# Performance work log

Hardware: AMD Instinct MI355X
Metric: run time of the kernel (lower is better)

Reference implementation:

```python
import jax, jax.numpy as jnp
import numpy as np

SUBSPACE_DIMS = np.array([1, 3, 3, 1])  # grade dims of 3D Clifford algebra (8 blades)
NUM_FEAT, NUM_HEADS, N_TOKENS, BS, C = 16, 8, 2048, 4, 8


def mv_linear(x, w, b):
    # x: [B, in, 8]; w: [out, in, 4] -> repeat over subspace dims -> [out, in, 8]
    wfull = jnp.repeat(w, SUBSPACE_DIMS, axis=-1)
    out = jnp.einsum('bic,oic->boc', x, wfull)
    return out.at[:, :, 0].add(b)  # bias on scalar blade only


def setup_inputs() -> dict:
    key = jax.random.key(0)
    ks = jax.random.split(key, 9)
    s = 0.05
    return {
        'feature_matrix': jax.random.normal(ks[0], (BS * N_TOKENS, NUM_FEAT, C), jnp.float32),
        'attention_mask': jnp.zeros((BS, N_TOKENS, N_TOKENS), jnp.float32),
        'wq': jax.random.normal(ks[1], (NUM_FEAT * NUM_HEADS, NUM_FEAT, 4), jnp.float32) * s,
        'bq': jax.random.normal(ks[2], (NUM_FEAT * NUM_HEADS,), jnp.float32) * s,
        'wk': jax.random.normal(ks[3], (NUM_FEAT * NUM_HEADS, NUM_FEAT, 4), jnp.float32) * s,
        'bk': jax.random.normal(ks[4], (NUM_FEAT * NUM_HEADS,), jnp.float32) * s,
        'wv': jax.random.normal(ks[5], (NUM_FEAT * NUM_HEADS, NUM_FEAT, 4), jnp.float32) * s,
        'bv': jax.random.normal(ks[6], (NUM_FEAT * NUM_HEADS,), jnp.float32) * s,
        'wo': jax.random.normal(ks[7], (NUM_FEAT, NUM_FEAT * NUM_HEADS, 4), jnp.float32) * s,
        'bo': jax.random.normal(ks[8], (NUM_FEAT,), jnp.float32) * s,
    }


def reference(feature_matrix, attention_mask, wq, bq, wk, bk, wv, bv, wo, bo):
    H, D = NUM_HEADS, NUM_FEAT
    n = N_TOKENS
    bs = feature_matrix.shape[0] // n

    def split_heads(t):  # [(bs n), (h d), c] -> [bs, h, n, d*c]
        return t.reshape(bs, n, H, D, C).transpose(0, 2, 1, 3, 4).reshape(bs, H, n, D * C)

    q = split_heads(mv_linear(feature_matrix, wq, bq)) / jnp.sqrt(jnp.float32(D * 8))
    k = split_heads(mv_linear(feature_matrix, wk, bk))
    v = split_heads(mv_linear(feature_matrix, wv, bv))

    attn = jnp.einsum('bhqe,bhke->bhqk', q, k) + attention_mask[:, None, :, :]
    attn = jax.nn.softmax(attn, axis=-1)
    out = jnp.einsum('bhqk,bhke->bhqe', attn, v)  # [bs, H, n, D*C]

    # transpose(1,2) then view(bs*n, H*D, 8)
    out = out.transpose(0, 2, 1, 3).reshape(bs * n, H * D, C)
    return mv_linear(out, wo, bo)
```

## Files before the change

kernel.cpp:

```cpp
#include <hip/hip_runtime.h>
#include <hip/hip_bf16.h>

typedef __attribute__((ext_vector_type(8))) __bf16 bf16x8;
typedef __attribute__((ext_vector_type(4))) float f32x4;
typedef __attribute__((ext_vector_type(8))) unsigned short ushort8;

#define TOKS 8192
#define LOG2E 1.4426950408889634f

__global__ __launch_bounds__(128) void proj_kernel(
    const float* __restrict__ x,
    const float* __restrict__ wq, const float* __restrict__ bq,
    const float* __restrict__ wk, const float* __restrict__ bk,
    const float* __restrict__ wv, const float* __restrict__ bv,
    __bf16* __restrict__ Qg, __bf16* __restrict__ Kg, __bf16* __restrict__ Vg)
{
    __shared__ float xs[512];
    const int tid = threadIdx.x;
    const int t0 = blockIdx.x * 4;
    ((float4*)xs)[tid] = ((const float4*)(x + (size_t)t0 * 128))[tid];
    __syncthreads();
    const int o = tid, h = o >> 4, d = o & 15;

    float acc[3][4][8];
#pragma unroll
    for (int tz = 0; tz < 3; ++tz) {
        const float bias = (tz == 0 ? bq : tz == 1 ? bk : bv)[o];
#pragma unroll
        for (int t = 0; t < 4; ++t) {
            acc[tz][t][0] = bias;
#pragma unroll
            for (int c = 1; c < 8; ++c) acc[tz][t][c] = 0.f;
        }
    }
    const float4* w40 = (const float4*)(wq + o * 64);
    const float4* w41 = (const float4*)(wk + o * 64);
    const float4* w42 = (const float4*)(wv + o * 64);
    for (int i = 0; i < 16; ++i) {
        float4 wv3[3] = {w40[i], w41[i], w42[i]};
#pragma unroll
        for (int t = 0; t < 4; ++t) {
            f32x4 xlo = *(const f32x4*)(xs + t * 128 + i * 8);
            f32x4 xhi = *(const f32x4*)(xs + t * 128 + i * 8 + 4);
            float xv[8] = {xlo[0], xlo[1], xlo[2], xlo[3],
                           xhi[0], xhi[1], xhi[2], xhi[3]};
#pragma unroll
            for (int tz = 0; tz < 3; ++tz) {
                float wr[8] = {wv3[tz].x, wv3[tz].y, wv3[tz].y, wv3[tz].y,
                               wv3[tz].z, wv3[tz].z, wv3[tz].z, wv3[tz].w};
#pragma unroll
                for (int c = 0; c < 8; ++c) acc[tz][t][c] += xv[c] * wr[c];
            }
        }
    }
    const int bb = t0 >> 11, tt0 = t0 & 2047;
    size_t base = (((size_t)(bb * 8 + h)) * 2048 + tt0) * 128 + d * 8;
#pragma unroll
    for (int tz = 0; tz < 3; ++tz) {
        __bf16* Og = tz == 0 ? Qg : tz == 1 ? Kg : Vg;
        const float scale = (tz == 0) ? 0.08838834764831845f : 1.0f;
#pragma unroll
        for (int t = 0; t < 4; ++t) {
            bf16x8 v;
#pragma unroll
            for (int c = 0; c < 8; ++c) v[c] = (__bf16)(acc[tz][t][c] * scale);
            *(bf16x8*)(Og + base + (size_t)t * 128) = v;
        }
    }
}

__global__ __launch_bounds__(256) void transv_kernel(
    const __bf16* __restrict__ Vg, __bf16* __restrict__ Vt)
{
    __shared__ __align__(16) char T[16384];
    const int tid = threadIdx.x;
    const int bh = blockIdx.y, t0 = blockIdx.x * 64;
    const __bf16* src = Vg + ((size_t)bh * 2048 + t0) * 128;
#pragma unroll
    for (int it = 0; it < 4; ++it) {
        int cidx = it * 256 + tid;
        int r = cidx >> 4, e0 = (cidx & 15) * 8;
        bf16x8 v = *(const bf16x8*)(src + r * 128 + e0);
        *(bf16x8*)(T + ((r * 256 + e0 * 2) ^ ((r & 7) << 4))) = v;
    }
    __syncthreads();
    const int e = tid & 127, half = tid >> 7;
    __bf16* dst = Vt + ((size_t)bh * 128 + e) * 2048 + t0 + half * 32;
#pragma unroll
    for (int jc = 0; jc < 4; ++jc) {
        ushort8 o8;
#pragma unroll
        for (int j = 0; j < 8; ++j) {
            int t = half * 32 + jc * 8 + j;
            o8[j] = *(const unsigned short*)(T + ((t * 256 + e * 2) ^ ((t & 7) << 4)));
        }
        *(ushort8*)(dst + jc * 8) = o8;
    }
}

__global__ __launch_bounds__(256) void flash_kernel(
    const __bf16* __restrict__ Qg, const __bf16* __restrict__ Kg,
    const __bf16* __restrict__ Vtg, const float* __restrict__ mask,
    __bf16* __restrict__ AO)
{
    __shared__ __align__(16) char Kl[16384];
    __shared__ __align__(16) char Vl[16384];
    __shared__ __align__(16) char Pl[8192];

    const int tid = threadIdx.x;
    const int lane = tid & 63, w = tid >> 6;
    const int l15 = lane & 15, lg = lane >> 4;
    const int bh = blockIdx.y, b = bh >> 3;
    const int q0 = blockIdx.x * 64;

    int kg[4], klb[4], vg[4], vlb[4];
#pragma unroll
    for (int it = 0; it < 4; ++it) {
        int cidx = it * 256 + tid;
        int kv = cidx >> 4, c15 = cidx & 15;
        kg[it] = kv * 128 + c15 * 8;
        klb[it] = kv * 256 + ((c15 * 16) ^ ((kv & 7) << 4));
        int e = cidx >> 3, j = cidx & 7;
        vg[it] = e * 2048 + j * 8;
        vlb[it] = e * 128 + ((j * 16) ^ ((e & 7) << 4));
    }
    const __bf16* kbase = Kg + (size_t)bh * 2048 * 128;
    const __bf16* vtbase = Vtg + (size_t)bh * 128 * 2048;
    const float* mbase = mask + ((size_t)b * 2048 + q0 + w * 16 + l15) * 2048;

    bf16x8 qf[4];
    {
        const __bf16* qp = Qg + ((size_t)bh * 2048 + q0 + w * 16 + l15) * 128 + lg * 8;
#pragma unroll
        for (int ks = 0; ks < 4; ++ks) qf[ks] = *(const bf16x8*)(qp + ks * 32);
    }

    f32x4 o_acc[8];
#pragma unroll
    for (int i = 0; i < 8; ++i) o_acc[i] = (f32x4){0.f, 0.f, 0.f, 0.f};
    float m = -1e30f, lsum = 0.f;
    const int pbase = w * 2048 + l15 * 128;
    const int psw = (l15 & 7) << 4;

    bf16x8 kreg[4], vreg[4];
#pragma unroll
    for (int it = 0; it < 4; ++it) {
        kreg[it] = *(const bf16x8*)(kbase + kg[it]);
        vreg[it] = *(const bf16x8*)(vtbase + vg[it]);
    }
#pragma unroll
    for (int it = 0; it < 4; ++it) {
        *(bf16x8*)(Kl + klb[it]) = kreg[it];
        *(bf16x8*)(Vl + vlb[it]) = vreg[it];
    }
    f32x4 mr[4];
#pragma unroll
    for (int ct = 0; ct < 4; ++ct)
        mr[ct] = *(const f32x4*)(mbase + ct * 16 + lg * 4);

    for (int kv0 = 0; kv0 < 2048; kv0 += 64) {
        __syncthreads();
        const bool more = (kv0 + 64) < 2048;
        if (more) {
            const __bf16* kb = kbase + (size_t)(kv0 + 64) * 128;
            const __bf16* vb = vtbase + (kv0 + 64);
#pragma unroll
            for (int it = 0; it < 4; ++it) {
                kreg[it] = *(const bf16x8*)(kb + kg[it]);
                vreg[it] = *(const bf16x8*)(vb + vg[it]);
            }
        }

        f32x4 st[4];
        __builtin_amdgcn_s_setprio(1);
#pragma unroll
        for (int ct = 0; ct < 4; ++ct) {
            f32x4 acc = (f32x4){0.f, 0.f, 0.f, 0.f};
            const int kvr = ct * 16 + l15;
            const int rowb = kvr * 256, sw = (kvr & 7) << 4;
#pragma unroll
            for (int ks = 0; ks < 4; ++ks) {
                bf16x8 kf = *(const bf16x8*)(Kl + rowb + ((ks * 64 + lg * 16) ^ sw));
                acc = __builtin_amdgcn_mfma_f32_16x16x32_bf16(kf, qf[ks], acc, 0, 0, 0);
            }
            st[ct] = acc;
        }
        __builtin_amdgcn_s_setprio(0);
#pragma unroll
        for (int ct = 0; ct < 4; ++ct)
#pragma unroll
            for (int r = 0; r < 4; ++r) st[ct][r] += mr[ct][r];

        float pmax = fmaxf(fmaxf(fmaxf(st[0][0], st[0][1]), fmaxf(st[0][2], st[0][3])),
                           fmaxf(fmaxf(st[1][0], st[1][1]), fmaxf(st[1][2], st[1][3])));
        pmax = fmaxf(pmax,
               fmaxf(fmaxf(fmaxf(st[2][0], st[2][1]), fmaxf(st[2][2], st[2][3])),
                     fmaxf(fmaxf(st[3][0], st[3][1]), fmaxf(st[3][2], st[3][3]))));
        pmax = fmaxf(pmax, __shfl_xor(pmax, 16));
        pmax = fmaxf(pmax, __shfl_xor(pmax, 32));

        if (!__all(pmax - m <= 6.0f)) {
            const float mnew = fmaxf(m, pmax);
            const float alpha = exp2f((m - mnew) * LOG2E);
            m = mnew;
            lsum *= alpha;
#pragma unroll
            for (int ct2 = 0; ct2 < 8; ++ct2)
#pragma unroll
                for (int r = 0; r < 4; ++r) o_acc[ct2][r] *= alpha;
        }

        float rsum = 0.f;
#pragma unroll
        for (int ct = 0; ct < 4; ++ct) {
            union { __bf16 h[4]; unsigned long long u64; } pk;
#pragma unroll
            for (int r = 0; r < 4; ++r) {
                float p = exp2f((st[ct][r] - m) * LOG2E);
                rsum += p;
                pk.h[r] = (__bf16)p;
            }
            *(unsigned long long*)(Pl + pbase + ((ct * 32 + lg * 8) ^ psw)) = pk.u64;
        }
        rsum += __shfl_xor(rsum, 16);
        rsum += __shfl_xor(rsum, 32);
        lsum += rsum;

        asm volatile("s_waitcnt lgkmcnt(0)" ::: "memory");
        __builtin_amdgcn_sched_barrier(0);

        __builtin_amdgcn_s_setprio(1);
#pragma unroll
        for (int ks2 = 0; ks2 < 2; ++ks2) {
            bf16x8 pf = *(const bf16x8*)(Pl + pbase + ((ks2 * 64 + lg * 16) ^ psw));
#pragma unroll
            for (int ct2 = 0; ct2 < 8; ++ct2) {
                const int e = ct2 * 16 + l15;
                bf16x8 vf = *(const bf16x8*)(Vl + e * 128 +
                                             ((ks2 * 64 + lg * 16) ^ ((e & 7) << 4)));
                o_acc[ct2] = __builtin_amdgcn_mfma_f32_16x16x32_bf16(vf, pf, o_acc[ct2], 0, 0, 0);
            }
        }
        __builtin_amdgcn_s_setprio(0);
        __syncthreads();

        if (more) {
#pragma unroll
            for (int it = 0; it < 4; ++it) {
                *(bf16x8*)(Kl + klb[it]) = kreg[it];
                *(bf16x8*)(Vl + vlb[it]) = vreg[it];
            }
#pragma unroll
            for (int ct = 0; ct < 4; ++ct)
                mr[ct] = *(const f32x4*)(mbase + kv0 + 64 + ct * 16 + lg * 4);
        }
    }

    const float linv = 1.0f / lsum;
    const size_t tok = (size_t)b * 2048 + q0 + w * 16 + l15;
    __bf16* aop = AO + tok * 1024 + (bh & 7) * 128;
#pragma unroll
    for (int ct2 = 0; ct2 < 8; ++ct2) {
        union { __bf16 h[4]; unsigned long long u64; } ov;
#pragma unroll
        for (int r = 0; r < 4; ++r) ov.h[r] = (__bf16)(o_acc[ct2][r] * linv);
        *(unsigned long long*)(aop + ct2 * 16 + lg * 4) = ov.u64;
    }
}

__global__ __launch_bounds__(128) void outproj_kernel(
    const __bf16* __restrict__ AO, const float* __restrict__ wo,
    const float* __restrict__ bo, float* __restrict__ out)
{
    __shared__ float al[8 * 1032];
    const int tid = threadIdx.x;
    const int t0 = blockIdx.x * 8;
#pragma unroll
    for (int it = 0; it < 8; ++it) {
        bf16x8 v = *(const bf16x8*)(AO + (size_t)(t0 + it) * 1024 + tid * 8);
        f32x4 lo = {(float)v[0], (float)v[1], (float)v[2], (float)v[3]};
        f32x4 hi = {(float)v[4], (float)v[5], (float)v[6], (float)v[7]};
        *(f32x4*)(al + it * 1032 + tid * 8) = lo;
        *(f32x4*)(al + it * 1032 + tid * 8 + 4) = hi;
    }
    __syncthreads();
    const int o = tid >> 3, t = tid & 7;
    float acc[8];
    acc[0] = bo[o];
#pragma unroll
    for (int c = 1; c < 8; ++c) acc[c] = 0.f;
    const float4* w4 = (const float4*)wo + o * 128;
    for (int ii = 0; ii < 128; ++ii) {
        float4 wv = w4[ii];
        f32x4 xlo = *(const f32x4*)(al + t * 1032 + ii * 8);
        f32x4 xhi = *(const f32x4*)(al + t * 1032 + ii * 8 + 4);
        float wr[8] = {wv.x, wv.y, wv.y, wv.y, wv.z, wv.z, wv.z, wv.w};
        float xv[8] = {xlo[0], xlo[1], xlo[2], xlo[3], xhi[0], xhi[1], xhi[2], xhi[3]};
#pragma unroll
        for (int c = 0; c < 8; ++c) acc[c] += xv[c] * wr[c];
    }
    float* op = out + (size_t)(t0 + t) * 128 + o * 8;
    *(float4*)op = (float4){acc[0], acc[1], acc[2], acc[3]};
    *(float4*)(op + 4) = (float4){acc[4], acc[5], acc[6], acc[7]};
}

extern "C" void kernel_launch(void* const* d_in, const int* in_sizes, int n_in,
                              void* d_out, int out_size, void* d_ws, size_t ws_size,
                              hipStream_t stream)
{
    const float* x    = (const float*)d_in[0];
    const float* mask = (const float*)d_in[1];
    const float* wq   = (const float*)d_in[2];
    const float* bq   = (const float*)d_in[3];
    const float* wk   = (const float*)d_in[4];
    const float* bk   = (const float*)d_in[5];
    const float* wv   = (const float*)d_in[6];
    const float* bv   = (const float*)d_in[7];
    const float* wo   = (const float*)d_in[8];
    const float* bo   = (const float*)d_in[9];
    float* out = (float*)d_out;

    const size_t SLOT = (size_t)32 * 2048 * 128;
    const size_t need = SLOT * 4 * 2;
    if (ws_size < need) {
        hipMemsetAsync(d_out, 0, (size_t)out_size * sizeof(float), stream);
        return;
    }
    __bf16* Qg = (__bf16*)d_ws;
    __bf16* Kg = Qg + SLOT;
    __bf16* Vg = Kg + SLOT;
    __bf16* Vt = Vg + SLOT;
    __bf16* AO = Vg;

    proj_kernel<<<TOKS / 4, 128, 0, stream>>>(x, wq, bq, wk, bk, wv, bv, Qg, Kg, Vg);
    transv_kernel<<<dim3(32, 32), 256, 0, stream>>>(Vg, Vt);
    flash_kernel<<<dim3(32, 32), 256, 0, stream>>>(Qg, Kg, Vt, mask, AO);
    outproj_kernel<<<TOKS / 8, 128, 0, stream>>>(AO, wo, bo, out);
}
```

Measured before the change: 200.6 us.

## Process two 16-row query tiles per wave in flash attention to reuse K/V tiles

Each wave now handles 32 query rows (two independent 16-row softmax states) instead of 16, so each block covers 128 queries and the grid halves. Every K and V fragment read from LDS feeds two MFMAs, halving the K/V global and LDS traffic per query. The mask prefetch moves from the end of the previous iteration to the top of each iteration. The cost is roughly double the accumulator registers, which lowers occupancy, and only 512 blocks are left to fill the GPU.

New measurement: 265.7 us. 1.32x slower.

```diff
diff --git a/kernel.cpp b/kernel.cpp
--- a/kernel.cpp
+++ b/kernel.cpp
@@ -105,13 +105,13 @@
 {
     __shared__ __align__(16) char Kl[16384];
     __shared__ __align__(16) char Vl[16384];
-    __shared__ __align__(16) char Pl[8192];
+    __shared__ __align__(16) char Pl[16384];
 
     const int tid = threadIdx.x;
     const int lane = tid & 63, w = tid >> 6;
     const int l15 = lane & 15, lg = lane >> 4;
     const int bh = blockIdx.y, b = bh >> 3;
-    const int q0 = blockIdx.x * 64;
+    const int q0 = blockIdx.x * 128;
 
     int kg[4], klb[4], vg[4], vlb[4];
 #pragma unroll
@@ -126,20 +126,29 @@
     }
     const __bf16* kbase = Kg + (size_t)bh * 2048 * 128;
     const __bf16* vtbase = Vtg + (size_t)bh * 128 * 2048;
-    const float* mbase = mask + ((size_t)b * 2048 + q0 + w * 16 + l15) * 2048;
-
-    bf16x8 qf[4];
+    const int qrow0 = q0 + w * 32 + l15;
+    const float* mbase0 = mask + ((size_t)b * 2048 + qrow0) * 2048;
+    const float* mbase1 = mbase0 + 16 * 2048;
+
+    bf16x8 qf0[4], qf1[4];
     {
-        const __bf16* qp = Qg + ((size_t)bh * 2048 + q0 + w * 16 + l15) * 128 + lg * 8;
-#pragma unroll
-        for (int ks = 0; ks < 4; ++ks) qf[ks] = *(const bf16x8*)(qp + ks * 32);
-    }
-
-    f32x4 o_acc[8];
-#pragma unroll
-    for (int i = 0; i < 8; ++i) o_acc[i] = (f32x4){0.f, 0.f, 0.f, 0.f};
-    float m = -1e30f, lsum = 0.f;
-    const int pbase = w * 2048 + l15 * 128;
+        const __bf16* qp = Qg + ((size_t)bh * 2048 + qrow0) * 128 + lg * 8;
+#pragma unroll
+        for (int ks = 0; ks < 4; ++ks) {
+            qf0[ks] = *(const bf16x8*)(qp + ks * 32);
+            qf1[ks] = *(const bf16x8*)(qp + 16 * 128 + ks * 32);
+        }
+    }
+
+    f32x4 o_acc0[8], o_acc1[8];
+#pragma unroll
+    for (int i = 0; i < 8; ++i) {
+        o_acc0[i] = (f32x4){0.f, 0.f, 0.f, 0.f};
+        o_acc1[i] = (f32x4){0.f, 0.f, 0.f, 0.f};
+    }
+    float m0 = -1e30f, lsum0 = 0.f, m1 = -1e30f, lsum1 = 0.f;
+    const int pbase0 = w * 4096 + l15 * 128;
+    const int pbase1 = pbase0 + 2048;
     const int psw = (l15 & 7) << 4;
 
     bf16x8 kreg[4], vreg[4];
@@ -153,14 +162,17 @@
         *(bf16x8*)(Kl + klb[it]) = kreg[it];
         *(bf16x8*)(Vl + vlb[it]) = vreg[it];
     }
-    f32x4 mr[4];
-#pragma unroll
-    for (int ct = 0; ct < 4; ++ct)
-        mr[ct] = *(const f32x4*)(mbase + ct * 16 + lg * 4);
 
     for (int kv0 = 0; kv0 < 2048; kv0 += 64) {
         __syncthreads();
         const bool more = (kv0 + 64) < 2048;
+
+        f32x4 mr0[4], mr1[4];
+#pragma unroll
+        for (int ct = 0; ct < 4; ++ct) {
+            mr0[ct] = *(const f32x4*)(mbase0 + kv0 + ct * 16 + lg * 4);
+            mr1[ct] = *(const f32x4*)(mbase1 + kv0 + ct * 16 + lg * 4);
+        }
         if (more) {
             const __bf16* kb = kbase + (size_t)(kv0 + 64) * 128;
             const __bf16* vb = vtbase + (kv0 + 64);
@@ -171,60 +183,96 @@
             }
         }
 
-        f32x4 st[4];
+        f32x4 st0[4], st1[4];
         __builtin_amdgcn_s_setprio(1);
 #pragma unroll
         for (int ct = 0; ct < 4; ++ct) {
-            f32x4 acc = (f32x4){0.f, 0.f, 0.f, 0.f};
+            f32x4 a0 = (f32x4){0.f, 0.f, 0.f, 0.f};
+            f32x4 a1 = (f32x4){0.f, 0.f, 0.f, 0.f};
             const int kvr = ct * 16 + l15;
             const int rowb = kvr * 256, sw = (kvr & 7) << 4;
 #pragma unroll
             for (int ks = 0; ks < 4; ++ks) {
                 bf16x8 kf = *(const bf16x8*)(Kl + rowb + ((ks * 64 + lg * 16) ^ sw));
-                acc = __builtin_amdgcn_mfma_f32_16x16x32_bf16(kf, qf[ks], acc, 0, 0, 0);
-            }
-            st[ct] = acc;
+                a0 = __builtin_amdgcn_mfma_f32_16x16x32_bf16(kf, qf0[ks], a0, 0, 0, 0);
+                a1 = __builtin_amdgcn_mfma_f32_16x16x32_bf16(kf, qf1[ks], a1, 0, 0, 0);
+            }
+            st0[ct] = a0; st1[ct] = a1;
         }
         __builtin_amdgcn_s_setprio(0);
+
 #pragma unroll
         for (int ct = 0; ct < 4; ++ct)
 #pragma unroll
-            for (int r = 0; r < 4; ++r) st[ct][r] += mr[ct][r];
-
-        float pmax = fmaxf(fmaxf(fmaxf(st[0][0], st[0][1]), fmaxf(st[0][2], st[0][3])),
-                           fmaxf(fmaxf(st[1][0], st[1][1]), fmaxf(st[1][2], st[1][3])));
-        pmax = fmaxf(pmax,
-               fmaxf(fmaxf(fmaxf(st[2][0], st[2][1]), fmaxf(st[2][2], st[2][3])),
-                     fmaxf(fmaxf(st[3][0], st[3][1]), fmaxf(st[3][2], st[3][3]))));
-        pmax = fmaxf(pmax, __shfl_xor(pmax, 16));
-        pmax = fmaxf(pmax, __shfl_xor(pmax, 32));
-
-        if (!__all(pmax - m <= 6.0f)) {
-            const float mnew = fmaxf(m, pmax);
-            const float alpha = exp2f((m - mnew) * LOG2E);
-            m = mnew;
-            lsum *= alpha;
-#pragma unroll
-            for (int ct2 = 0; ct2 < 8; ++ct2)
-#pragma unroll
-                for (int r = 0; r < 4; ++r) o_acc[ct2][r] *= alpha;
-        }
-
-        float rsum = 0.f;
-#pragma unroll
-        for (int ct = 0; ct < 4; ++ct) {
-            union { __bf16 h[4]; unsigned long long u64; } pk;
-#pragma unroll
-            for (int r = 0; r < 4; ++r) {
-                float p = exp2f((st[ct][r] - m) * LOG2E);
-                rsum += p;
-                pk.h[r] = (__bf16)p;
-            }
-            *(unsigned long long*)(Pl + pbase + ((ct * 32 + lg * 8) ^ psw)) = pk.u64;
-        }
-        rsum += __shfl_xor(rsum, 16);
-        rsum += __shfl_xor(rsum, 32);
-        lsum += rsum;
+            for (int r = 0; r < 4; ++r) st0[ct][r] += mr0[ct][r];
+        {
+            float pmax = fmaxf(fmaxf(fmaxf(st0[0][0], st0[0][1]), fmaxf(st0[0][2], st0[0][3])),
+                               fmaxf(fmaxf(st0[1][0], st0[1][1]), fmaxf(st0[1][2], st0[1][3])));
+            pmax = fmaxf(pmax,
+                   fmaxf(fmaxf(fmaxf(st0[2][0], st0[2][1]), fmaxf(st0[2][2], st0[2][3])),
+                         fmaxf(fmaxf(st0[3][0], st0[3][1]), fmaxf(st0[3][2], st0[3][3]))));
+            pmax = fmaxf(pmax, __shfl_xor(pmax, 16));
+            pmax = fmaxf(pmax, __shfl_xor(pmax, 32));
+            if (!__all(pmax - m0 <= 6.0f)) {
+                const float mnew = fmaxf(m0, pmax);
+                const float alpha = exp2f((m0 - mnew) * LOG2E);
+                m0 = mnew; lsum0 *= alpha;
+#pragma unroll
+                for (int i = 0; i < 8; ++i)
+#pragma unroll
+                    for (int r = 0; r < 4; ++r) o_acc0[i][r] *= alpha;
+            }
+            float rsum = 0.f;
+#pragma unroll
+            for (int ct = 0; ct < 4; ++ct) {
+                union { __bf16 h[4]; unsigned long long u64; } pk;
+#pragma unroll
+                for (int r = 0; r < 4; ++r) {
+                    float p = exp2f((st0[ct][r] - m0) * LOG2E);
+                    rsum += p; pk.h[r] = (__bf16)p;
+                }
+                *(unsigned long long*)(Pl + pbase0 + ((ct * 32 + lg * 8) ^ psw)) = pk.u64;
+            }
+            rsum += __shfl_xor(rsum, 16);
+            rsum += __shfl_xor(rsum, 32);
+            lsum0 += rsum;
+        }
+#pragma unroll
+        for (int ct = 0; ct < 4; ++ct)
+#pragma unroll
+            for (int r = 0; r < 4; ++r) st1[ct][r] += mr1[ct][r];
+        {
+            float pmax = fmaxf(fmaxf(fmaxf(st1[0][0], st1[0][1]), fmaxf(st1[0][2], st1[0][3])),
+                               fmaxf(fmaxf(st1[1][0], st1[1][1]), fmaxf(st1[1][2], st1[1][3])));
+            pmax = fmaxf(pmax,
+                   fmaxf(fmaxf(fmaxf(st1[2][0], st1[2][1]), fmaxf(st1[2][2], st1[2][3])),
+                         fmaxf(fmaxf(st1[3][0], st1[3][1]), fmaxf(st1[3][2], st1[3][3]))));
+            pmax = fmaxf(pmax, __shfl_xor(pmax, 16));
+            pmax = fmaxf(pmax, __shfl_xor(pmax, 32));
+            if (!__all(pmax - m1 <= 6.0f)) {
+                const float mnew = fmaxf(m1, pmax);
+                const float alpha = exp2f((m1 - mnew) * LOG2E);
+                m1 = mnew; lsum1 *= alpha;
+#pragma unroll
+                for (int i = 0; i < 8; ++i)
+#pragma unroll
+                    for (int r = 0; r < 4; ++r) o_acc1[i][r] *= alpha;
+            }
+            float rsum = 0.f;
+#pragma unroll
+            for (int ct = 0; ct < 4; ++ct) {
+                union { __bf16 h[4]; unsigned long long u64; } pk;
+#pragma unroll
+                for (int r = 0; r < 4; ++r) {
+                    float p = exp2f((st1[ct][r] - m1) * LOG2E);
+                    rsum += p; pk.h[r] = (__bf16)p;
+                }
+                *(unsigned long long*)(Pl + pbase1 + ((ct * 32 + lg * 8) ^ psw)) = pk.u64;
+            }
+            rsum += __shfl_xor(rsum, 16);
+            rsum += __shfl_xor(rsum, 32);
+            lsum1 += rsum;
+        }
 
         asm volatile("s_waitcnt lgkmcnt(0)" ::: "memory");
         __builtin_amdgcn_sched_barrier(0);
@@ -232,13 +280,15 @@
         __builtin_amdgcn_s_setprio(1);
 #pragma unroll
         for (int ks2 = 0; ks2 < 2; ++ks2) {
-            bf16x8 pf = *(const bf16x8*)(Pl + pbase + ((ks2 * 64 + lg * 16) ^ psw));
+            bf16x8 pf0 = *(const bf16x8*)(Pl + pbase0 + ((ks2 * 64 + lg * 16) ^ psw));
+            bf16x8 pf1 = *(const bf16x8*)(Pl + pbase1 + ((ks2 * 64 + lg * 16) ^ psw));
 #pragma unroll
             for (int ct2 = 0; ct2 < 8; ++ct2) {
                 const int e = ct2 * 16 + l15;
                 bf16x8 vf = *(const bf16x8*)(Vl + e * 128 +
                                              ((ks2 * 64 + lg * 16) ^ ((e & 7) << 4)));
-                o_acc[ct2] = __builtin_amdgcn_mfma_f32_16x16x32_bf16(vf, pf, o_acc[ct2], 0, 0, 0);
+                o_acc0[ct2] = __builtin_amdgcn_mfma_f32_16x16x32_bf16(vf, pf0, o_acc0[ct2], 0, 0, 0);
+                o_acc1[ct2] = __builtin_amdgcn_mfma_f32_16x16x32_bf16(vf, pf1, o_acc1[ct2], 0, 0, 0);
             }
         }
         __builtin_amdgcn_s_setprio(0);
@@ -250,21 +300,30 @@
                 *(bf16x8*)(Kl + klb[it]) = kreg[it];
                 *(bf16x8*)(Vl + vlb[it]) = vreg[it];
             }
-#pragma unroll
-            for (int ct = 0; ct < 4; ++ct)
-                mr[ct] = *(const f32x4*)(mbase + kv0 + 64 + ct * 16 + lg * 4);
-        }
-    }
-
-    const float linv = 1.0f / lsum;
-    const size_t tok = (size_t)b * 2048 + q0 + w * 16 + l15;
-    __bf16* aop = AO + tok * 1024 + (bh & 7) * 128;
-#pragma unroll
-    for (int ct2 = 0; ct2 < 8; ++ct2) {
-        union { __bf16 h[4]; unsigned long long u64; } ov;
-#pragma unroll
-        for (int r = 0; r < 4; ++r) ov.h[r] = (__bf16)(o_acc[ct2][r] * linv);
-        *(unsigned long long*)(aop + ct2 * 16 + lg * 4) = ov.u64;
+        }
+    }
+
+    {
+        const float linv = 1.0f / lsum0;
+        __bf16* aop = AO + ((size_t)b * 2048 + qrow0) * 1024 + (bh & 7) * 128;
+#pragma unroll
+        for (int ct2 = 0; ct2 < 8; ++ct2) {
+            union { __bf16 h[4]; unsigned long long u64; } ov;
+#pragma unroll
+            for (int r = 0; r < 4; ++r) ov.h[r] = (__bf16)(o_acc0[ct2][r] * linv);
+            *(unsigned long long*)(aop + ct2 * 16 + lg * 4) = ov.u64;
+        }
+    }
+    {
+        const float linv = 1.0f / lsum1;
+        __bf16* aop = AO + ((size_t)b * 2048 + qrow0 + 16) * 1024 + (bh & 7) * 128;
+#pragma unroll
+        for (int ct2 = 0; ct2 < 8; ++ct2) {
+            union { __bf16 h[4]; unsigned long long u64; } ov;
+#pragma unroll
+            for (int r = 0; r < 4; ++r) ov.h[r] = (__bf16)(o_acc1[ct2][r] * linv);
+            *(unsigned long long*)(aop + ct2 * 16 + lg * 4) = ov.u64;
+        }
     }
 }
 
@@ -334,6 +393,6 @@
 
     proj_kernel<<<TOKS / 4, 128, 0, stream>>>(x, wq, bq, wk, bk, wv, bv, Qg, Kg, Vg);
     transv_kernel<<<dim3(32, 32), 256, 0, stream>>>(Vg, Vt);
-    flash_kernel<<<dim3(32, 32), 256, 0, stream>>>(Qg, Kg, Vt, mask, AO);
+    flash_kernel<<<dim3(16, 32), 256, 0, stream>>>(Qg, Kg, Vt, mask, AO);
     outproj_kernel<<<TOKS / 8, 128, 0, stream>>>(AO, wo, bo, out);
 }
```
